# Optimization experiments

Measured on AMD Instinct MI355X. Metric: run time of the kernel, lower is better.

## Reference

```python
import jax, jax.numpy as jnp
import numpy as np

EPS = 1e-5
PATCH_LEN, STRIDE, SEQ_LEN = 16, 8, 512
D_FF, N_HEADS = 32, 8


def setup_inputs() -> dict:
    key = jax.random.key(0)
    ks = jax.random.split(key, 16)
    d_model, d_llm, V, num_tok, pred_len = 32, 4096, 32000, 1000, 96
    hf = N_HEADS * D_FF  # 256
    patch_nums = (SEQ_LEN - PATCH_LEN) // STRIDE + 2  # 64
    head_nf = D_FF * patch_nums  # 2048
    r = lambda k, s, fan: jax.random.normal(k, s, jnp.float32) / np.sqrt(fan)
    return {
        'x_enc': jax.random.normal(ks[0], (32, SEQ_LEN, 7), jnp.float32),
        'conv_w': r(ks[1], (d_model, PATCH_LEN, 3), PATCH_LEN * 3),
        'word_emb': jax.random.normal(ks[2], (V, d_llm), jnp.float32) * 0.02,
        'map_w': r(ks[3], (num_tok, V), V),
        'map_b': jnp.zeros((num_tok,), jnp.float32),
        'wq': r(ks[4], (hf, d_model), d_model), 'bq': jnp.zeros((hf,), jnp.float32),
        'wk': r(ks[5], (hf, d_llm), d_llm), 'bk': jnp.zeros((hf,), jnp.float32),
        'wv': r(ks[6], (hf, d_llm), d_llm), 'bv': jnp.zeros((hf,), jnp.float32),
        'wo': r(ks[7], (d_llm, hf), hf), 'bo': jnp.zeros((d_llm,), jnp.float32),
        'head_w': r(ks[8], (pred_len, head_nf), head_nf),
        'head_b': jnp.zeros((pred_len,), jnp.float32),
    }


def _forward(x_enc, conv_w, word_emb, map_w, map_b, wq, bq, wk, bk, wv, bv, wo, bo, head_w, head_b):
    B, T, N = x_enc.shape
    # RevIN normalize (stats detached, as in torch)
    mean = jax.lax.stop_gradient(jnp.mean(x_enc, axis=1, keepdims=True))
    stdev = jax.lax.stop_gradient(jnp.sqrt(jnp.var(x_enc, axis=1, keepdims=True) + EPS))
    x = (x_enc - mean) / stdev                      # [B,T,N]

    # Patch embedding: [B,N,T] -> replication pad -> unfold -> circular conv
    xt = jnp.transpose(x, (0, 2, 1))                # [B,N,T]
    xt = jnp.concatenate([xt, jnp.repeat(xt[..., -1:], STRIDE, axis=-1)], axis=-1)  # [B,N,T+stride]
    starts = jnp.arange(0, T + STRIDE - PATCH_LEN + 1, STRIDE)
    idx = starts[:, None] + jnp.arange(PATCH_LEN)   # [L, patch_len]
    patches = xt[:, :, idx]                         # [B,N,L,patch_len]
    L = patches.shape[2]
    p = patches.reshape(B * N, L, PATCH_LEN)
    # TokenEmbedding: conv1d over patch axis, circular pad 1, no bias
    pc = jnp.transpose(p, (0, 2, 1))                # [BN, patch_len, L]
    pc = jnp.concatenate([pc[..., -1:], pc, pc[..., :1]], axis=-1)
    emb = jax.lax.conv_general_dilated(pc, conv_w, (1,), 'VALID',
                                       dimension_numbers=('NCH', 'OIH', 'NCH'))
    enc = jnp.transpose(emb, (0, 2, 1))             # [BN, L, d_model]

    # Source embeddings: mapping_layer(word_emb.T).T -> [num_tokens, d_llm]
    src = (word_emb.T @ map_w.T + map_b).T          # [num_tok, d_llm]

    # Reprogramming cross-attention
    BN = enc.shape[0]
    q = (enc @ wq.T + bq).reshape(BN, L, N_HEADS, D_FF)   # [BN,L,H,E]
    k = (src @ wk.T + bk).reshape(-1, N_HEADS, D_FF)      # [S,H,E]
    v = (src @ wv.T + bv).reshape(-1, N_HEADS, D_FF)      # [S,H,E]
    scale = 1.0 / np.sqrt(D_FF)
    scores = jnp.einsum('blhe,she->bhls', q, k)
    A = jax.nn.softmax(scale * scores, axis=-1)
    rep = jnp.einsum('bhls,she->blhe', A, v).reshape(BN, L, N_HEADS * D_FF)
    out = rep @ wo.T + bo                           # [BN, L, d_llm]

    # LLM stubbed as identity; keep first d_ff channels (Time-LLM post-LLM path)
    dec = out[..., :D_FF]                           # [BN, L, d_ff]
    dec = dec.reshape(B, N, L, D_FF).transpose(0, 1, 3, 2)  # [B,N,d_ff,L]
    dec = dec.reshape(B, N, D_FF * L)               # FlattenHead
    dec = dec @ head_w.T + head_b                   # [B,N,pred_len]
    dec = jnp.transpose(dec, (0, 2, 1))             # [B,pred_len,N]
    # RevIN denormalize
    return dec * stdev + mean


def reference(x_enc, conv_w, word_emb, map_w, map_b, wq, bq, wk, bk, wv, bv, wo, bo, head_w, head_b):
    return _forward(x_enc, conv_w, word_emb, map_w, map_b, wq, bq, wk, bk, wv, bv, wo, bo, head_w, head_b)
```

## Files before the change

### kernel.cpp

```cpp
#include <hip/hip_runtime.h>
#include <math.h>

constexpr int B_ = 32, T_ = 512, N_ = 7, BN_ = 224;
constexpr int L_ = 64, DM_ = 32, PLEN_ = 16;
constexpr int HF_ = 256, NH_ = 8, DFF_ = 32;
constexpr int S_ = 1000, SP_ = 1024, DLLM_ = 4096, V_ = 32000;
constexpr int PRED_ = 96, HNF_ = 2048;
constexpr int KSPLIT2 = 25, KCH2 = 1280;

typedef short bf16x8 __attribute__((ext_vector_type(8)));
typedef float f32x4 __attribute__((ext_vector_type(4)));

__device__ inline ushort f2bf(float x) {
    union { float f; uint u; } v; v.f = x;
    uint r = v.u + 0x7fffu + ((v.u >> 16) & 1u);
    return (ushort)(r >> 16);
}
__device__ inline uint pk(float a, float b) {
    return (uint)f2bf(a) | ((uint)f2bf(b) << 16);
}
__device__ inline void gl16(const void* g, void* l) {
    __builtin_amdgcn_global_load_lds(
        (const __attribute__((address_space(1))) void*)g,
        (__attribute__((address_space(3))) void*)l, 16, 0, 0);
}

__global__ __launch_bounds__(256) void k_stats(const float* __restrict__ x,
                                               float* __restrict__ mean_o,
                                               float* __restrict__ std_o) {
    int bn = blockIdx.x, b = bn / N_, n = bn % N_;
    const float* xp = x + (size_t)b * T_ * N_ + n;
    float s = 0.f, sq = 0.f;
    for (int t = threadIdx.x; t < T_; t += 256) { float v = xp[(size_t)t * N_]; s += v; sq += v * v; }
    for (int o = 32; o > 0; o >>= 1) { s += __shfl_down(s, o, 64); sq += __shfl_down(sq, o, 64); }
    __shared__ float rs[4], rq[4];
    int wid = threadIdx.x >> 6, lane = threadIdx.x & 63;
    if (lane == 0) { rs[wid] = s; rq[wid] = sq; }
    __syncthreads();
    if (threadIdx.x == 0) {
        float S = rs[0] + rs[1] + rs[2] + rs[3];
        float Q = rq[0] + rq[1] + rq[2] + rq[3];
        float m = S / T_;
        float var = Q / T_ - m * m;
        mean_o[bn] = m;
        std_o[bn] = sqrtf(var + 1e-5f);
    }
}

__global__ __launch_bounds__(256) void k_wsum(const float* __restrict__ wk,
                                              const float* __restrict__ wv,
                                              float* __restrict__ wsum) {
    int c = blockIdx.x;
    const float* row = (c < HF_) ? wk + (size_t)c * DLLM_ : wv + (size_t)(c - HF_) * DLLM_;
    float s = 0.f;
    for (int d = threadIdx.x; d < DLLM_; d += 256) s += row[d];
    for (int o = 32; o > 0; o >>= 1) s += __shfl_down(s, o, 64);
    __shared__ float rs[4];
    int wid = threadIdx.x >> 6, lane = threadIdx.x & 63;
    if (lane == 0) rs[wid] = s;
    __syncthreads();
    if (threadIdx.x == 0) wsum[c] = rs[0] + rs[1] + rs[2] + rs[3];
}

__global__ __launch_bounds__(256) void k_enc(const float* __restrict__ x,
                                             const float* __restrict__ conv_w,
                                             const float* __restrict__ mean_i,
                                             const float* __restrict__ std_i,
                                             float* __restrict__ enc) {
    int bn = blockIdx.x, b = bn / N_, n = bn % N_;
    __shared__ float xn[520];
    __shared__ float cw[DM_ * PLEN_ * 3];
    float m = mean_i[bn], rstd = 1.0f / std_i[bn];
    for (int i = threadIdx.x; i < DM_ * PLEN_ * 3; i += 256) cw[i] = conv_w[i];
    const float* xp = x + (size_t)b * T_ * N_ + n;
    for (int t = threadIdx.x; t < T_; t += 256) xn[t] = (xp[(size_t)t * N_] - m) * rstd;
    __syncthreads();
    if (threadIdx.x < 8) xn[T_ + threadIdx.x] = xn[T_ - 1];
    __syncthreads();
    for (int idx = threadIdx.x; idx < L_ * DM_; idx += 256) {
        int l = idx >> 5, o = idx & 31;
        float acc = 0.f;
        #pragma unroll
        for (int t = 0; t < 3; t++) {
            int col = l + t;
            int pcol = (col == 0) ? 63 : ((col == 65) ? 0 : col - 1);
            const float* xb = &xn[pcol * 8];
            const float* cwb = &cw[o * 48 + t];
            #pragma unroll
            for (int i = 0; i < 16; i++) acc += xb[i] * cwb[i * 3];
        }
        enc[(size_t)bn * 2048 + idx] = acc;
    }
}

__global__ __launch_bounds__(256) void k_q(const float* __restrict__ enc,
                                           const float* __restrict__ wq,
                                           const float* __restrict__ bq,
                                           float* __restrict__ qo) {
    int bn = blockIdx.x;
    __shared__ float et[2048];
    __shared__ float wqs[HF_ * DM_];
    for (int i = threadIdx.x; i < 2048; i += 256) et[i] = enc[(size_t)bn * 2048 + i];
    for (int i = threadIdx.x; i < HF_ * DM_; i += 256) wqs[i] = wq[i];
    __syncthreads();
    const float scale = 0.17677669529663687f;
    for (int idx = threadIdx.x; idx < L_ * HF_; idx += 256) {
        int l = idx >> 8, c = idx & 255;
        float acc = bq[c];
        const float* e = &et[l * 32];
        const float* w = &wqs[c * 32];
        #pragma unroll
        for (int k = 0; k < 32; k++) acc += e[k] * w[k];
        qo[(size_t)bn * L_ * HF_ + idx] = acc * scale;
    }
}

__global__ __launch_bounds__(256) void k_cvt_wkv(const float* __restrict__ wk,
                                                 const float* __restrict__ wv,
                                                 ushort* __restrict__ out) {
    int g = blockIdx.x * 256 + threadIdx.x;
    int e = g * 8;
    const float* src = (e < HF_ * DLLM_) ? wk + e : wv + (e - HF_ * DLLM_);
    float4 x = *(const float4*)src, y = *(const float4*)(src + 4);
    uint4 w; w.x = pk(x.x, x.y); w.y = pk(x.z, x.w); w.z = pk(y.x, y.y); w.w = pk(y.z, y.w);
    *(uint4*)(out + e) = w;
}

__global__ __launch_bounds__(512) void k_gemm1(const float* __restrict__ A,
                                               const ushort* __restrict__ Bw,
                                               ushort* __restrict__ ET) {
    __shared__ union {
        struct { ushort A[2][128 * 32]; ushort B[2][256 * 32]; } st;
        ushort C[256 * 72];
    } lds;
    const int tid = threadIdx.x;
    const int lane = tid & 63, wid = tid >> 6;
    const int wr = wid >> 2, wc = wid & 3;
    const int n0 = blockIdx.x * 256, m0 = blockIdx.y * 128;

    const int ar = tid >> 2, ao = tid & 3;
    const int au = (ar << 2) | (ao ^ ((ar >> 1) & 3));
    const float* aptr = A + (size_t)(m0 + ar) * DLLM_ + ao * 8;

    const int u0 = tid, rb0 = u0 >> 2, ob0 = (u0 & 3) ^ ((rb0 >> 1) & 3);
    const int u1 = tid + 512, rb1 = u1 >> 2, ob1 = (u1 & 3) ^ ((rb1 >> 1) & 3);
    const ushort* bptr0 = Bw + (size_t)(n0 + rb0) * DLLM_ + ob0 * 8;
    const ushort* bptr1 = Bw + (size_t)(n0 + rb1) * DLLM_ + ob1 * 8;

    const int rl = lane & 15;
    const int oc = (lane >> 4) ^ ((rl >> 1) & 3);

    f32x4 acc[4][4];
    #pragma unroll
    for (int i = 0; i < 4; i++)
        #pragma unroll
        for (int j = 0; j < 4; j++) acc[i][j] = (f32x4){0.f, 0.f, 0.f, 0.f};

    {
        gl16(bptr0, &lds.st.B[0][u0 * 8]);
        gl16(bptr1, &lds.st.B[0][u1 * 8]);
        float4 a0 = *(const float4*)aptr;
        float4 a1 = *(const float4*)(aptr + 4);
        uint4 wa; wa.x = pk(a0.x, a0.y); wa.y = pk(a0.z, a0.w); wa.z = pk(a1.x, a1.y); wa.w = pk(a1.z, a1.w);
        *(uint4*)&lds.st.A[0][au * 8] = wa;
    }
    __syncthreads();

    int cur = 0;
    constexpr int NT = DLLM_ / 32;
    for (int t = 0; t < NT; ++t) {
        const bool more = (t + 1 < NT);
        float4 a0, a1;
        if (more) {
            const int o = (t + 1) * 32;
            gl16(bptr0 + o, &lds.st.B[cur ^ 1][u0 * 8]);
            gl16(bptr1 + o, &lds.st.B[cur ^ 1][u1 * 8]);
            const float* ap = aptr + o;
            a0 = *(const float4*)ap; a1 = *(const float4*)(ap + 4);
        }
        const ushort* Ab = lds.st.A[cur];
        const ushort* Bb = lds.st.B[cur];
        bf16x8 af[4], bfr[4];
        #pragma unroll
        for (int mi = 0; mi < 4; mi++)
            af[mi] = *(const bf16x8*)&Ab[(wr * 64 + mi * 16 + rl) * 32 + oc * 8];
        #pragma unroll
        for (int ni = 0; ni < 4; ni++)
            bfr[ni] = *(const bf16x8*)&Bb[(wc * 64 + ni * 16 + rl) * 32 + oc * 8];
        #pragma unroll
        for (int mi = 0; mi < 4; mi++)
            #pragma unroll
            for (int ni = 0; ni < 4; ni++)
                acc[mi][ni] = __builtin_amdgcn_mfma_f32_16x16x32_bf16(af[mi], bfr[ni], acc[mi][ni], 0, 0, 0);
        if (more) {
            uint4 wa; wa.x = pk(a0.x, a0.y); wa.y = pk(a0.z, a0.w); wa.z = pk(a1.x, a1.y); wa.w = pk(a1.z, a1.w);
            *(uint4*)&lds.st.A[cur ^ 1][au * 8] = wa;
        }
        __syncthreads();
        cur ^= 1;
    }

    #pragma unroll
    for (int p = 0; p < 2; p++) {
        __syncthreads();
        if (wr == p) {
            #pragma unroll
            for (int mi = 0; mi < 4; mi++)
                #pragma unroll
                for (int ni = 0; ni < 4; ni++) {
                    int nl = wc * 64 + ni * 16 + (lane & 15);
                    int ml = mi * 16 + (lane >> 4) * 4;
                    uint2 w2;
                    w2.x = pk(acc[mi][ni][0], acc[mi][ni][1]);
                    w2.y = pk(acc[mi][ni][2], acc[mi][ni][3]);
                    *(uint2*)&lds.C[nl * 72 + ml] = w2;
                }
        }
        __syncthreads();
        {
            int r = tid >> 1, half = tid & 1;
            const uint4* src = (const uint4*)&lds.C[r * 72 + half * 32];
            ushort* dst = ET + (size_t)(n0 + r) * V_ + m0 + p * 64 + half * 32;
            uint4 v0 = src[0], v1 = src[1], v2 = src[2], v3 = src[3];
            *(uint4*)(dst + 0) = v0; *(uint4*)(dst + 8) = v1;
            *(uint4*)(dst + 16) = v2; *(uint4*)(dst + 24) = v3;
        }
    }
}

__global__ __launch_bounds__(256) void k_gemm2(const float* __restrict__ A,
                                               const ushort* __restrict__ ET,
                                               float* __restrict__ Cp) {
    __shared__ float Af[2][128 * 32];
    __shared__ ushort Bs[2][128 * 32];
    const int tid = threadIdx.x, lane = tid & 63, wid = tid >> 6;
    const int wr = wid >> 1, wc = wid & 1;
    const int m0 = blockIdx.x * 128, n0 = blockIdx.y * 128, kz = blockIdx.z;
    const size_t kbase = (size_t)kz * KCH2;

    const float* asrc[4];
    #pragma unroll
    for (int i = 0; i < 4; i++) {
        int u = i * 256 + tid;
        int r = u >> 3, c = (u & 7) ^ (r & 7);
        int rm = m0 + r; if (rm > S_ - 1) rm = S_ - 1;
        asrc[i] = A + (size_t)rm * V_ + kbase + c * 4;
    }
    const int u0 = tid, rb0 = u0 >> 2, ob0 = (u0 & 3) ^ ((rb0 >> 1) & 3);
    const int u1 = tid + 256, rb1 = u1 >> 2, ob1 = (u1 & 3) ^ ((rb1 >> 1) & 3);
    const ushort* bp0 = ET + (size_t)(n0 + rb0) * V_ + kbase + ob0 * 8;
    const ushort* bp1 = ET + (size_t)(n0 + rb1) * V_ + kbase + ob1 * 8;

    const int rl = lane & 15;
    const int oB = (lane >> 4) ^ ((rl >> 1) & 3);
    const int oA = lane >> 4;

    f32x4 acc[4][4];
    #pragma unroll
    for (int i = 0; i < 4; i++)
        #pragma unroll
        for (int j = 0; j < 4; j++) acc[i][j] = (f32x4){0.f, 0.f, 0.f, 0.f};

    {
        gl16(bp0, &Bs[0][u0 * 8]);
        gl16(bp1, &Bs[0][u1 * 8]);
        #pragma unroll
        for (int i = 0; i < 4; i++) gl16(asrc[i], &Af[0][(i * 256 + tid) * 4]);
    }
    __syncthreads();

    int cur = 0;
    constexpr int NT = KCH2 / 32;
    for (int t = 0; t < NT; ++t) {
        const bool more = (t + 1 < NT);
        if (more) {
            const int o = (t + 1) * 32;
            gl16(bp0 + o, &Bs[cur ^ 1][u0 * 8]);
            gl16(bp1 + o, &Bs[cur ^ 1][u1 * 8]);
            #pragma unroll
            for (int i = 0; i < 4; i++) gl16(asrc[i] + o, &Af[cur ^ 1][(i * 256 + tid) * 4]);
        }
        const float* Ab = Af[cur];
        const ushort* Bb = Bs[cur];
        bf16x8 af[4], bfr[4];
        #pragma unroll
        for (int mi = 0; mi < 4; mi++) {
            int row = wr * 64 + mi * 16 + rl;
            int s = row & 7;
            int ulo = row * 8 + ((2 * oA) ^ s);
            int uhi = row * 8 + ((2 * oA + 1) ^ s);
            f32x4 xlo = *(const f32x4*)&Ab[ulo * 4];
            f32x4 xhi = *(const f32x4*)&Ab[uhi * 4];
            uint4 w; w.x = pk(xlo[0], xlo[1]); w.y = pk(xlo[2], xlo[3]);
            w.z = pk(xhi[0], xhi[1]); w.w = pk(xhi[2], xhi[3]);
            union { uint4 u; bf16x8 b; } cv; cv.u = w;
            af[mi] = cv.b;
        }
        #pragma unroll
        for (int ni = 0; ni < 4; ni++)
            bfr[ni] = *(const bf16x8*)&Bb[(wc * 64 + ni * 16 + rl) * 32 + oB * 8];
        #pragma unroll
        for (int mi = 0; mi < 4; mi++)
            #pragma unroll
            for (int ni = 0; ni < 4; ni++)
                acc[mi][ni] = __builtin_amdgcn_mfma_f32_16x16x32_bf16(af[mi], bfr[ni], acc[mi][ni], 0, 0, 0);
        __syncthreads();
        cur ^= 1;
    }

    #pragma unroll
    for (int mi = 0; mi < 4; mi++)
        #pragma unroll
        for (int ni = 0; ni < 4; ni++)
            #pragma unroll
            for (int j = 0; j < 4; j++) {
                int m = m0 + wr * 64 + mi * 16 + (lane >> 4) * 4 + j;
                int n = n0 + wc * 64 + ni * 16 + (lane & 15);
                if (m < S_) Cp[((size_t)kz * S_ + m) * 512 + n] = acc[mi][ni][j];
            }
}

__global__ __launch_bounds__(256) void k_red(const float* __restrict__ Cp,
                                             const float* __restrict__ mb,
                                             const float* __restrict__ wsum,
                                             const float* __restrict__ bk,
                                             const float* __restrict__ bv,
                                             ushort* __restrict__ Kb,
                                             ushort* __restrict__ Vt) {
    int idx = blockIdx.x * 256 + threadIdx.x;
    if (idx >= SP_ * 512) return;
    int m = idx >> 9, n = idx & 511;
    float s = 0.f;
    if (m < S_) {
        #pragma unroll
        for (int z = 0; z < KSPLIT2; z++) s += Cp[(size_t)z * S_ * 512 + (size_t)m * 512 + n];
        float bias = (n < HF_) ? bk[n] : bv[n - HF_];
        s += mb[m] * wsum[n] + bias;
    }
    ushort h = f2bf(s);
    if (n < HF_) Kb[(size_t)m * HF_ + n] = h;
    else Vt[(size_t)(n - HF_) * SP_ + m] = h;
}

__global__ __launch_bounds__(256) void k_attn(const float* __restrict__ q,
                                              const ushort* __restrict__ Kb,
                                              const ushort* __restrict__ Vt,
                                              float* __restrict__ rep) {
    const int h = blockIdx.x, bn = blockIdx.y;
    __shared__ ushort Ks[64 * 32];
    __shared__ ushort Vs[32 * 64];
    __shared__ float  Ps[4][16 * 64];
    const int tid = threadIdx.x, lane = tid & 63, w = tid >> 6;
    const int rl = lane & 15, g = lane >> 4;

    const int krow = tid >> 2, koc = (tid & 3) ^ ((krow >> 1) & 3);
    const ushort* ksrc = Kb + (size_t)krow * HF_ + h * 32 + koc * 8;
    ushort* kdst = &Ks[tid * 8];
    const int verow = tid >> 3, vso = (tid & 7) ^ (verow & 7);
    const ushort* vsrc = Vt + (size_t)(h * 32 + verow) * SP_ + vso * 8;
    ushort* vdst = &Vs[tid * 8];

    bf16x8 qf;
    {
        const float* qp = q + ((size_t)bn * L_ + w * 16 + rl) * HF_ + h * 32 + g * 8;
        float4 x = *(const float4*)qp, y = *(const float4*)(qp + 4);
        uint4 u; u.x = pk(x.x, x.y); u.y = pk(x.z, x.w); u.z = pk(y.x, y.y); u.w = pk(y.z, y.w);
        union { uint4 u4; bf16x8 b; } cv; cv.u4 = u; qf = cv.b;
    }

    float mrow[4] = {-1e30f, -1e30f, -1e30f, -1e30f};
    float rsum[4] = {0.f, 0.f, 0.f, 0.f};
    f32x4 oacc[2] = {(f32x4){0,0,0,0}, (f32x4){0,0,0,0}};
    float* Pw = Ps[w];

    for (int t = 0; t < 16; ++t) {
        const int s0 = t * 64;
        gl16(ksrc + (size_t)s0 * HF_, kdst);
        gl16(vsrc + s0, vdst);
        __syncthreads();

        f32x4 sc[4];
        #pragma unroll
        for (int nf = 0; nf < 4; nf++) {
            const int row = nf * 16 + rl;
            bf16x8 kf = *(const bf16x8*)&Ks[(row * 4 + (g ^ ((rl >> 1) & 3))) * 8];
            sc[nf] = __builtin_amdgcn_mfma_f32_16x16x32_bf16(qf, kf, (f32x4){0, 0, 0, 0}, 0, 0, 0);
            if (s0 + row >= S_) sc[nf] = (f32x4){-1e30f, -1e30f, -1e30f, -1e30f};
        }
        float tmax[4];
        #pragma unroll
        for (int j = 0; j < 4; j++)
            tmax[j] = fmaxf(fmaxf(sc[0][j], sc[1][j]), fmaxf(sc[2][j], sc[3][j]));
        #pragma unroll
        for (int d = 1; d < 16; d <<= 1)
            #pragma unroll
            for (int j = 0; j < 4; j++) tmax[j] = fmaxf(tmax[j], __shfl_xor(tmax[j], d, 64));
        float resc[4];
        #pragma unroll
        for (int j = 0; j < 4; j++) {
            float mn = fmaxf(mrow[j], tmax[j]);
            resc[j] = __expf(mrow[j] - mn);
            mrow[j] = mn;
            rsum[j] *= resc[j];
            oacc[0][j] *= resc[j];
            oacc[1][j] *= resc[j];
        }
        #pragma unroll
        for (int nf = 0; nf < 4; nf++) {
            const int s = nf * 16 + rl;
            #pragma unroll
            for (int j = 0; j < 4; j++) {
                float p = __expf(sc[nf][j] - mrow[j]);
                float pf = __uint_as_float(((uint)f2bf(p)) << 16);
                rsum[j] += pf;
                const int row = 4 * g + j;
                Pw[row * 64 + (((s >> 2) ^ row) << 2) + (s & 3)] = pf;
            }
        }
        #pragma unroll
        for (int h2 = 0; h2 < 2; h2++) {
            const int q1 = (h2 * 8 + 2 * g) ^ rl;
            const int q2 = (h2 * 8 + 2 * g + 1) ^ rl;
            f32x4 plo = *(const f32x4*)&Pw[rl * 64 + q1 * 4];
            f32x4 phi = *(const f32x4*)&Pw[rl * 64 + q2 * 4];
            uint4 pu; pu.x = pk(plo[0], plo[1]); pu.y = pk(plo[2], plo[3]);
            pu.z = pk(phi[0], phi[1]); pu.w = pk(phi[2], phi[3]);
            union { uint4 u; bf16x8 b; } cv; cv.u = pu;
            bf16x8 pa = cv.b;
            #pragma unroll
            for (int eg = 0; eg < 2; eg++) {
                const int erow = eg * 16 + rl;
                const int su = (h2 * 4 + g) ^ (erow & 7);
                bf16x8 vf = *(const bf16x8*)&Vs[erow * 64 + su * 8];
                oacc[eg] = __builtin_amdgcn_mfma_f32_16x16x32_bf16(pa, vf, oacc[eg], 0, 0, 0);
            }
        }
        __syncthreads();
    }

    #pragma unroll
    for (int d = 1; d < 16; d <<= 1)
        #pragma unroll
        for (int j = 0; j < 4; j++) rsum[j] += __shfl_xor(rsum[j], d, 64);
    float inv[4];
    #pragma unroll
    for (int j = 0; j < 4; j++) inv[j] = 1.0f / rsum[j];
    #pragma unroll
    for (int eg = 0; eg < 2; eg++)
        #pragma unroll
        for (int j = 0; j < 4; j++)
            rep[((size_t)bn * HF_ + h * 32 + eg * 16 + rl) * 64 + w * 16 + 4 * g + j] =
                oacc[eg][j] * inv[j];
}

__global__ __launch_bounds__(256) void k_out(const float* __restrict__ rep,
                                             const float* __restrict__ wo,
                                             const float* __restrict__ bo,
                                             float* __restrict__ out32) {
    const int bn = blockIdx.x;
    __shared__ float woT[HF_][32];
    const int tid = threadIdx.x;
    for (int idx = tid; idx < HF_ * 32; idx += 256) {
        int e = idx & 31, c = idx >> 5;
        woT[c][e] = wo[(size_t)e * HF_ + c];
    }
    __syncthreads();
    const int l = tid & 63, e0 = (tid >> 6) * 8;
    float acc[8];
    #pragma unroll
    for (int i = 0; i < 8; i++) acc[i] = bo[e0 + i];
    const float* rp = rep + (size_t)bn * HF_ * 64 + l;
    for (int c = 0; c < HF_; c++) {
        float rv = rp[(size_t)c * 64];
        #pragma unroll
        for (int i = 0; i < 8; i++) acc[i] += rv * woT[c][e0 + i];
    }
    float* op = out32 + ((size_t)bn * L_ + l) * 32 + e0;
    #pragma unroll
    for (int i = 0; i < 8; i++) op[i] = acc[i];
}

__global__ __launch_bounds__(256) void k_head(const float* __restrict__ out32,
                                              const float* __restrict__ hw,
                                              const float* __restrict__ hb,
                                              const float* __restrict__ mean_i,
                                              const float* __restrict__ std_i,
                                              float* __restrict__ out) {
    int bn = blockIdx.x, b = bn / N_, n = bn % N_;
    __shared__ float dt[2048];
    for (int i = threadIdx.x; i < 2048; i += 256) dt[i] = out32[(size_t)bn * 2048 + i];
    __syncthreads();
    float m = mean_i[bn], sd = std_i[bn];
    for (int p = threadIdx.x; p < PRED_; p += 256) {
        float acc = hb[p];
        const float* w = hw + (size_t)p * HNF_;
        for (int f = 0; f < DFF_; f++) {
            const float* wf = w + f * 64;
            #pragma unroll
            for (int ll = 0; ll < 64; ll++) acc += dt[ll * 32 + f] * wf[ll];
        }
        out[(size_t)b * PRED_ * N_ + (size_t)p * N_ + n] = acc * sd + m;
    }
}

extern "C" void kernel_launch(void* const* d_in, const int* in_sizes, int n_in,
                              void* d_out, int out_size, void* d_ws, size_t ws_size,
                              hipStream_t stream) {
    const float* x_enc   = (const float*)d_in[0];
    const float* conv_w  = (const float*)d_in[1];
    const float* word_emb= (const float*)d_in[2];
    const float* map_w   = (const float*)d_in[3];
    const float* map_b   = (const float*)d_in[4];
    const float* wq      = (const float*)d_in[5];
    const float* bq      = (const float*)d_in[6];
    const float* wk      = (const float*)d_in[7];
    const float* bk      = (const float*)d_in[8];
    const float* wv      = (const float*)d_in[9];
    const float* bv      = (const float*)d_in[10];
    const float* wo      = (const float*)d_in[11];
    const float* bo      = (const float*)d_in[12];
    const float* head_w  = (const float*)d_in[13];
    const float* head_b  = (const float*)d_in[14];

    float* ws = (float*)d_ws;
    float* mean_w = ws;
    float* std_w  = ws + 256;
    float* wsum_w = ws + 512;
    float* enc_w  = ws + 1024;
    float* q_w    = enc_w + (size_t)BN_ * 2048;
    float* kv_w   = q_w + (size_t)BN_ * L_ * HF_;
    float* o32_w  = kv_w + (size_t)S_ * 512;
    float* cp_w   = o32_w + (size_t)BN_ * 2048;
    float* rep_w  = cp_w;
    ushort* et_w  = (ushort*)(cp_w + (size_t)KSPLIT2 * S_ * 512);
    ushort* wkv_w = et_w + (size_t)512 * V_;
    ushort* kb_w  = (ushort*)kv_w;
    ushort* vt_w  = kb_w + (size_t)SP_ * HF_;

    k_stats<<<BN_, 256, 0, stream>>>(x_enc, mean_w, std_w);
    k_wsum<<<512, 256, 0, stream>>>(wk, wv, wsum_w);
    k_enc<<<BN_, 256, 0, stream>>>(x_enc, conv_w, mean_w, std_w, enc_w);
    k_q<<<BN_, 256, 0, stream>>>(enc_w, wq, bq, q_w);
    k_cvt_wkv<<<(512 * DLLM_ / 8) / 256, 256, 0, stream>>>(wk, wv, wkv_w);
    k_gemm1<<<dim3(2, V_ / 128), 512, 0, stream>>>(word_emb, wkv_w, et_w);
    k_gemm2<<<dim3(8, 4, KSPLIT2), 256, 0, stream>>>(map_w, et_w, cp_w);
    k_red<<<(SP_ * 512) / 256, 256, 0, stream>>>(cp_w, map_b, wsum_w, bk, bv, kb_w, vt_w);
    k_attn<<<dim3(NH_, BN_), 256, 0, stream>>>(q_w, kb_w, vt_w, rep_w);
    k_out<<<BN_, 256, 0, stream>>>(rep_w, wo, bo, o32_w);
    k_head<<<BN_, 256, 0, stream>>>(o32_w, head_w, head_b, mean_w, std_w, (float*)d_out);
}
```

Before: 560.7 us.

## Stream fp32 A tiles directly to LDS and split barriers with explicit vmcnt waits

In gemm1, the fp32 A operand is now loaded asynchronously into LDS with global_load_lds, using the same XOR-swizzled layout as gemm2. It is converted to bf16 when fragments are read, rather than passing through registers and being converted before the LDS store. Both GEMM loops replace __syncthreads with explicit vmcnt/lgkmcnt waits plus raw s_barrier, so the next tile's prefetch can stay in flight while the current tile is computed. s_setprio raises wave priority around the MFMA blocks in the GEMMs and attention. The cost is a doubled A LDS footprint in gemm1 and hand-tuned waitcnt counts that must match the number of issued loads.

```diff
diff --git a/kernel.cpp b/kernel.cpp
--- a/kernel.cpp
+++ b/kernel.cpp
@@ -130,7 +130,7 @@
                                                const ushort* __restrict__ Bw,
                                                ushort* __restrict__ ET) {
     __shared__ union {
-        struct { ushort A[2][128 * 32]; ushort B[2][256 * 32]; } st;
+        struct { float Af[2][128 * 32]; ushort Bs[2][256 * 32]; } st;
         ushort C[256 * 72];
     } lds;
     const int tid = threadIdx.x;
@@ -138,17 +138,17 @@
     const int wr = wid >> 2, wc = wid & 3;
     const int n0 = blockIdx.x * 256, m0 = blockIdx.y * 128;
 
-    const int ar = tid >> 2, ao = tid & 3;
-    const int au = (ar << 2) | (ao ^ ((ar >> 1) & 3));
-    const float* aptr = A + (size_t)(m0 + ar) * DLLM_ + ao * 8;
+    const int arw = tid >> 3, acq = (tid & 7) ^ ((tid >> 3) & 7);
+    const float* asrc0 = A + (size_t)(m0 + arw) * DLLM_ + acq * 4;
+    const float* asrc1 = asrc0 + (size_t)64 * DLLM_;
 
     const int u0 = tid, rb0 = u0 >> 2, ob0 = (u0 & 3) ^ ((rb0 >> 1) & 3);
     const int u1 = tid + 512, rb1 = u1 >> 2, ob1 = (u1 & 3) ^ ((rb1 >> 1) & 3);
     const ushort* bptr0 = Bw + (size_t)(n0 + rb0) * DLLM_ + ob0 * 8;
     const ushort* bptr1 = Bw + (size_t)(n0 + rb1) * DLLM_ + ob1 * 8;
 
-    const int rl = lane & 15;
-    const int oc = (lane >> 4) ^ ((rl >> 1) & 3);
+    const int rl = lane & 15, g = lane >> 4;
+    const int oc = g ^ ((rl >> 1) & 3);
 
     f32x4 acc[4][4];
     #pragma unroll
@@ -156,47 +156,55 @@
         #pragma unroll
         for (int j = 0; j < 4; j++) acc[i][j] = (f32x4){0.f, 0.f, 0.f, 0.f};
 
-    {
-        gl16(bptr0, &lds.st.B[0][u0 * 8]);
-        gl16(bptr1, &lds.st.B[0][u1 * 8]);
-        float4 a0 = *(const float4*)aptr;
-        float4 a1 = *(const float4*)(aptr + 4);
-        uint4 wa; wa.x = pk(a0.x, a0.y); wa.y = pk(a0.z, a0.w); wa.z = pk(a1.x, a1.y); wa.w = pk(a1.z, a1.w);
-        *(uint4*)&lds.st.A[0][au * 8] = wa;
-    }
+    gl16(asrc0, &lds.st.Af[0][tid * 4]);
+    gl16(asrc1, &lds.st.Af[0][(tid + 512) * 4]);
+    gl16(bptr0, &lds.st.Bs[0][u0 * 8]);
+    gl16(bptr1, &lds.st.Bs[0][u1 * 8]);
     __syncthreads();
 
     int cur = 0;
     constexpr int NT = DLLM_ / 32;
     for (int t = 0; t < NT; ++t) {
-        const bool more = (t + 1 < NT);
-        float4 a0, a1;
-        if (more) {
+        if (t + 1 < NT) {
             const int o = (t + 1) * 32;
-            gl16(bptr0 + o, &lds.st.B[cur ^ 1][u0 * 8]);
-            gl16(bptr1 + o, &lds.st.B[cur ^ 1][u1 * 8]);
-            const float* ap = aptr + o;
-            a0 = *(const float4*)ap; a1 = *(const float4*)(ap + 4);
-        }
-        const ushort* Ab = lds.st.A[cur];
-        const ushort* Bb = lds.st.B[cur];
+            gl16(asrc0 + o, &lds.st.Af[cur ^ 1][tid * 4]);
+            gl16(asrc1 + o, &lds.st.Af[cur ^ 1][(tid + 512) * 4]);
+            gl16(bptr0 + o, &lds.st.Bs[cur ^ 1][u0 * 8]);
+            gl16(bptr1 + o, &lds.st.Bs[cur ^ 1][u1 * 8]);
+            asm volatile("s_waitcnt vmcnt(4)" ::: "memory");
+        } else {
+            asm volatile("s_waitcnt vmcnt(0)" ::: "memory");
+        }
+        __builtin_amdgcn_s_barrier();
+        asm volatile("" ::: "memory");
+        const float* Ab = lds.st.Af[cur];
+        const ushort* Bb = lds.st.Bs[cur];
         bf16x8 af[4], bfr[4];
         #pragma unroll
-        for (int mi = 0; mi < 4; mi++)
-            af[mi] = *(const bf16x8*)&Ab[(wr * 64 + mi * 16 + rl) * 32 + oc * 8];
+        for (int mi = 0; mi < 4; mi++) {
+            int row = wr * 64 + mi * 16 + rl;
+            int s = row & 7;
+            int ulo = row * 8 + ((2 * g) ^ s);
+            int uhi = row * 8 + ((2 * g + 1) ^ s);
+            f32x4 xlo = *(const f32x4*)&Ab[ulo * 4];
+            f32x4 xhi = *(const f32x4*)&Ab[uhi * 4];
+            uint4 w; w.x = pk(xlo[0], xlo[1]); w.y = pk(xlo[2], xlo[3]);
+            w.z = pk(xhi[0], xhi[1]); w.w = pk(xhi[2], xhi[3]);
+            union { uint4 u; bf16x8 b; } cv; cv.u = w;
+            af[mi] = cv.b;
+        }
         #pragma unroll
         for (int ni = 0; ni < 4; ni++)
             bfr[ni] = *(const bf16x8*)&Bb[(wc * 64 + ni * 16 + rl) * 32 + oc * 8];
+        __builtin_amdgcn_s_setprio(1);
         #pragma unroll
         for (int mi = 0; mi < 4; mi++)
             #pragma unroll
             for (int ni = 0; ni < 4; ni++)
                 acc[mi][ni] = __builtin_amdgcn_mfma_f32_16x16x32_bf16(af[mi], bfr[ni], acc[mi][ni], 0, 0, 0);
-        if (more) {
-            uint4 wa; wa.x = pk(a0.x, a0.y); wa.y = pk(a0.z, a0.w); wa.z = pk(a1.x, a1.y); wa.w = pk(a1.z, a1.w);
-            *(uint4*)&lds.st.A[cur ^ 1][au * 8] = wa;
-        }
-        __syncthreads();
+        __builtin_amdgcn_s_setprio(0);
+        asm volatile("s_waitcnt lgkmcnt(0)" ::: "memory");
+        __builtin_amdgcn_s_barrier();
         cur ^= 1;
     }
 
@@ -251,9 +259,8 @@
     const ushort* bp0 = ET + (size_t)(n0 + rb0) * V_ + kbase + ob0 * 8;
     const ushort* bp1 = ET + (size_t)(n0 + rb1) * V_ + kbase + ob1 * 8;
 
-    const int rl = lane & 15;
-    const int oB = (lane >> 4) ^ ((rl >> 1) & 3);
-    const int oA = lane >> 4;
+    const int rl = lane & 15, g = lane >> 4;
+    const int oB = g ^ ((rl >> 1) & 3);
 
     f32x4 acc[4][4];
     #pragma unroll
@@ -261,25 +268,27 @@
         #pragma unroll
         for (int j = 0; j < 4; j++) acc[i][j] = (f32x4){0.f, 0.f, 0.f, 0.f};
 
-    {
-        gl16(bp0, &Bs[0][u0 * 8]);
-        gl16(bp1, &Bs[0][u1 * 8]);
-        #pragma unroll
-        for (int i = 0; i < 4; i++) gl16(asrc[i], &Af[0][(i * 256 + tid) * 4]);
-    }
+    gl16(bp0, &Bs[0][u0 * 8]);
+    gl16(bp1, &Bs[0][u1 * 8]);
+    #pragma unroll
+    for (int i = 0; i < 4; i++) gl16(asrc[i], &Af[0][(i * 256 + tid) * 4]);
     __syncthreads();
 
     int cur = 0;
     constexpr int NT = KCH2 / 32;
     for (int t = 0; t < NT; ++t) {
-        const bool more = (t + 1 < NT);
-        if (more) {
+        if (t + 1 < NT) {
             const int o = (t + 1) * 32;
             gl16(bp0 + o, &Bs[cur ^ 1][u0 * 8]);
             gl16(bp1 + o, &Bs[cur ^ 1][u1 * 8]);
             #pragma unroll
             for (int i = 0; i < 4; i++) gl16(asrc[i] + o, &Af[cur ^ 1][(i * 256 + tid) * 4]);
-        }
+            asm volatile("s_waitcnt vmcnt(6)" ::: "memory");
+        } else {
+            asm volatile("s_waitcnt vmcnt(0)" ::: "memory");
+        }
+        __builtin_amdgcn_s_barrier();
+        asm volatile("" ::: "memory");
         const float* Ab = Af[cur];
         const ushort* Bb = Bs[cur];
         bf16x8 af[4], bfr[4];
@@ -287,8 +296,8 @@
         for (int mi = 0; mi < 4; mi++) {
             int row = wr * 64 + mi * 16 + rl;
             int s = row & 7;
-            int ulo = row * 8 + ((2 * oA) ^ s);
-            int uhi = row * 8 + ((2 * oA + 1) ^ s);
+            int ulo = row * 8 + ((2 * g) ^ s);
+            int uhi = row * 8 + ((2 * g + 1) ^ s);
             f32x4 xlo = *(const f32x4*)&Ab[ulo * 4];
             f32x4 xhi = *(const f32x4*)&Ab[uhi * 4];
             uint4 w; w.x = pk(xlo[0], xlo[1]); w.y = pk(xlo[2], xlo[3]);
@@ -299,12 +308,15 @@
         #pragma unroll
         for (int ni = 0; ni < 4; ni++)
             bfr[ni] = *(const bf16x8*)&Bb[(wc * 64 + ni * 16 + rl) * 32 + oB * 8];
+        __builtin_amdgcn_s_setprio(1);
         #pragma unroll
         for (int mi = 0; mi < 4; mi++)
             #pragma unroll
             for (int ni = 0; ni < 4; ni++)
                 acc[mi][ni] = __builtin_amdgcn_mfma_f32_16x16x32_bf16(af[mi], bfr[ni], acc[mi][ni], 0, 0, 0);
-        __syncthreads();
+        __builtin_amdgcn_s_setprio(0);
+        asm volatile("s_waitcnt lgkmcnt(0)" ::: "memory");
+        __builtin_amdgcn_s_barrier();
         cur ^= 1;
     }
 
@@ -380,6 +392,7 @@
         __syncthreads();
 
         f32x4 sc[4];
+        __builtin_amdgcn_s_setprio(1);
         #pragma unroll
         for (int nf = 0; nf < 4; nf++) {
             const int row = nf * 16 + rl;
@@ -387,6 +400,7 @@
             sc[nf] = __builtin_amdgcn_mfma_f32_16x16x32_bf16(qf, kf, (f32x4){0, 0, 0, 0}, 0, 0, 0);
             if (s0 + row >= S_) sc[nf] = (f32x4){-1e30f, -1e30f, -1e30f, -1e30f};
         }
+        __builtin_amdgcn_s_setprio(0);
         float tmax[4];
         #pragma unroll
         for (int j = 0; j < 4; j++)
@@ -417,6 +431,7 @@
                 Pw[row * 64 + (((s >> 2) ^ row) << 2) + (s & 3)] = pf;
             }
         }
+        __builtin_amdgcn_s_setprio(1);
         #pragma unroll
         for (int h2 = 0; h2 < 2; h2++) {
             const int q1 = (h2 * 8 + 2 * g) ^ rl;
@@ -435,6 +450,7 @@
                 oacc[eg] = __builtin_amdgcn_mfma_f32_16x16x32_bf16(pa, vf, oacc[eg], 0, 0, 0);
             }
         }
+        __builtin_amdgcn_s_setprio(0);
         __syncthreads();
     }
 
```

Result: faster. 532.3 us (-5.1%).
